# Performance work log

Measured on AMD Instinct MI355X. Metric: run time of the kernel, lower is better.

Reference implementation:

```python
import jax, jax.numpy as jnp
import numpy as np

TYPE_PANEL, TYPE_DIALOG, TYPE_CHAR = 1, 2, 3
NUM_ELEMS = 64  # max element index per type (panel count cap per page)
B, S, D = 8, 4096, 768
NPC, NDS = 4, 4  # num_panel_classes, num_dialog_shapes


def setup_inputs() -> dict:
    key = jax.random.key(0)
    ks = jax.random.split(key, 16)
    w = lambda k, shp: jax.random.normal(k, shp, dtype=jnp.float32) * 0.02
    return {
        "element_types": jax.random.randint(ks[0], (B, S), 0, 4, dtype=jnp.int32),
        "element_indices": jax.random.randint(ks[1], (B, S), 0, NUM_ELEMS, dtype=jnp.int32),
        "parent_panel_indices": jax.random.randint(ks[2], (B, S), 0, NUM_ELEMS, dtype=jnp.int32),
        "style_vector": jax.random.normal(ks[3], (B, 4), dtype=jnp.float32),
        "type_emb": w(ks[4], (4, D)),
        "index_emb": w(ks[5], (NUM_ELEMS, D)),
        "parent_emb": w(ks[6], (NUM_ELEMS, D)),
        "style_w": w(ks[7], (4, D)),
        "style_b": jnp.zeros((D,), jnp.float32),
        "ln_g": jnp.ones((D,), jnp.float32),
        "ln_b": jnp.zeros((D,), jnp.float32),
        "panel_w": w(ks[8], (D, NPC + 4)),
        "panel_b": jnp.zeros((NPC + 4,), jnp.float32),
        "dialog_w": w(ks[9], (2 * D, NDS + 4)),
        "dialog_b": jnp.zeros((NDS + 4,), jnp.float32),
        "char_w": w(ks[10], (2 * D, 4)),
        "char_b": jnp.zeros((4,), jnp.float32),
    }


def reference(element_types, element_indices, parent_panel_indices, style_vector,
              type_emb, index_emb, parent_emb, style_w, style_b, ln_g, ln_b,
              panel_w, panel_b, dialog_w, dialog_b, char_w, char_b):
    Bv, Sv = element_types.shape
    # --- TokenLayoutEncoder: embedding sum + style projection + LayerNorm ---
    x = type_emb[element_types] + index_emb[element_indices] + parent_emb[parent_panel_indices]
    x = x + (style_vector @ style_w + style_b)[:, None, :]
    mu = x.mean(-1, keepdims=True)
    var = ((x - mu) ** 2).mean(-1, keepdims=True)
    feats = (x - mu) * jax.lax.rsqrt(var + 1e-5) * ln_g + ln_b  # (B,S,D)

    # --- vectorized _build_parent_remap: orig panel idx -> kept panel order pos ---
    panel_mask = element_types == TYPE_PANEL                      # (B,S)
    kept = (jnp.cumsum(panel_mask, axis=1) - 1).astype(jnp.int32) # order pos of each panel token
    brow = jnp.arange(Bv, dtype=jnp.int32)[:, None]
    col = jnp.where(panel_mask, element_indices, NUM_ELEMS)       # dummy slot for non-panels
    remap = (jnp.full((Bv, NUM_ELEMS + 1), -1, jnp.int32)
             .at[brow, col].max(kept))[:, :NUM_ELEMS]             # (B, NUM_ELEMS)
    # kept panel order pos -> sequence position (for parent feature gather)
    slot = jnp.where(panel_mask, kept, Sv)
    seq_ids = jnp.broadcast_to(jnp.arange(Sv, dtype=jnp.int32), (Bv, Sv))
    pos_table = (jnp.zeros((Bv, Sv + 1), jnp.int32)
                 .at[brow, slot].set(seq_ids))[:, :Sv]            # (B,S)

    # --- parent_pos per token (DIALOG/CHAR only), -1 otherwise ---
    child_mask = (element_types == TYPE_DIALOG) | (element_types == TYPE_CHAR)
    ppos = jnp.where(child_mask,
                     jnp.take_along_axis(remap, parent_panel_indices, axis=1), -1)
    valid = ppos >= 0
    pseq = jnp.take_along_axis(pos_table, jnp.clip(ppos, 0, Sv - 1), axis=1)
    parent_feats = jnp.take_along_axis(feats, pseq[..., None], axis=1)
    parent_feats = parent_feats * valid[..., None].astype(feats.dtype)
    cat = jnp.concatenate([feats, parent_feats], axis=-1)         # (B,S,2D)

    # --- ParallelPredictionHeads, masked per token type ---
    panel_out = (feats @ panel_w + panel_b) * panel_mask[..., None].astype(feats.dtype)
    dmask = ((element_types == TYPE_DIALOG) & valid)[..., None].astype(feats.dtype)
    cmask = ((element_types == TYPE_CHAR) & valid)[..., None].astype(feats.dtype)
    dialog_out = (cat @ dialog_w + dialog_b) * dmask
    char_out = (cat @ char_w + char_b) * cmask
    return panel_out, dialog_out, char_out
```

## Files before the change

### kernel.cpp

```cpp
#include <hip/hip_runtime.h>

#define NB 8
#define NS 4096
#define ND 768

typedef float4 f4;

static __device__ __forceinline__ float wred(float v) {
    v += __shfl_xor(v, 32, 64);
    v += __shfl_xor(v, 16, 64);
    v += __shfl_xor(v, 8, 64);
    v += __shfl_xor(v, 4, 64);
    v += __shfl_xor(v, 2, 64);
    v += __shfl_xor(v, 1, 64);
    return v;
}

static __device__ __forceinline__ f4 ld4(const float* __restrict__ p, int i) {
    return ((const f4*)p)[i];
}

__global__ __launch_bounds__(256) void lp_pre(
    const int* __restrict__ et, const int* __restrict__ ei,
    const float* __restrict__ sv, const float* __restrict__ sw,
    const float* __restrict__ sb,
    int* __restrict__ table, float* __restrict__ sprj)
{
    if (blockIdx.x < 128) {
        int t = blockIdx.x * 256 + threadIdx.x;
        if (et[t] == 1) {
            int b = t >> 12;
            atomicMax(&table[b * 64 + ei[t]], t & (NS - 1));
        }
    } else {
        const int lane = threadIdx.x & 63;
        const int b = (blockIdx.x - 128) * 4 + (threadIdx.x >> 6);
        const float sv0 = sv[b*4+0], sv1 = sv[b*4+1], sv2 = sv[b*4+2], sv3 = sv[b*4+3];
        #pragma unroll
        for (int g = 0; g < 3; ++g) {
            int i = g*64 + lane;
            f4 w0 = ld4(sw, i), w1 = ld4(sw, 192+i), w2 = ld4(sw, 384+i), w3 = ld4(sw, 576+i);
            f4 bb = ld4(sb, i);
            f4 r;
            r.x = bb.x + sv0*w0.x + sv1*w1.x + sv2*w2.x + sv3*w3.x;
            r.y = bb.y + sv0*w0.y + sv1*w1.y + sv2*w2.y + sv3*w3.y;
            r.z = bb.z + sv0*w0.z + sv1*w1.z + sv2*w2.z + sv3*w3.z;
            r.w = bb.w + sv0*w0.w + sv1*w1.w + sv2*w2.w + sv3*w3.w;
            ((f4*)(sprj + b*ND))[i] = r;
        }
    }
}

__global__ __launch_bounds__(256) void lp_parent(
    const int* __restrict__ ei, const int* __restrict__ ppi,
    const float* __restrict__ temb, const float* __restrict__ iemb,
    const float* __restrict__ pemb, const float* __restrict__ lng,
    const float* __restrict__ lnb,
    const int* __restrict__ table, const float* __restrict__ sprj,
    float* __restrict__ pfeat)
{
    const int lane = threadIdx.x & 63;
    const int slot = blockIdx.x * 4 + (threadIdx.x >> 6);
    const int b = slot >> 6;
    const int pp = table[slot];
    if (pp < 0) return;
    const int ptok = b * NS + pp;
    const int pei = ei[ptok], pppi = ppi[ptok];
    const float* ie = iemb + pei * ND;
    const float* pe = pemb + pppi * ND;
    const float* sp = sprj + b * ND;

    f4 x[3]; float s1 = 0.f;
    #pragma unroll
    for (int g = 0; g < 3; ++g) {
        int i = g*64 + lane;
        f4 a = ld4(temb + ND, i), c = ld4(ie, i), d = ld4(pe, i), s = ld4(sp, i);
        x[g].x = a.x + c.x + d.x + s.x;
        x[g].y = a.y + c.y + d.y + s.y;
        x[g].z = a.z + c.z + d.z + s.z;
        x[g].w = a.w + c.w + d.w + s.w;
        s1 += x[g].x + x[g].y + x[g].z + x[g].w;
    }
    float mu = wred(s1) * (1.f/ND);
    float s2 = 0.f;
    #pragma unroll
    for (int g = 0; g < 3; ++g) {
        float dx = x[g].x-mu, dy = x[g].y-mu, dz = x[g].z-mu, dw_ = x[g].w-mu;
        s2 += dx*dx + dy*dy + dz*dz + dw_*dw_;
    }
    float rs = rsqrtf(wred(s2) * (1.f/ND) + 1e-5f);
    float* dst = pfeat + (size_t)slot * ND;
    #pragma unroll
    for (int g = 0; g < 3; ++g) {
        int i = g*64 + lane;
        f4 gg = ld4(lng, i), bb = ld4(lnb, i);
        f4 r;
        r.x = (x[g].x-mu)*rs*gg.x + bb.x;
        r.y = (x[g].y-mu)*rs*gg.y + bb.y;
        r.z = (x[g].z-mu)*rs*gg.z + bb.z;
        r.w = (x[g].w-mu)*rs*gg.w + bb.w;
        ((f4*)dst)[i] = r;
    }
}

__global__ __launch_bounds__(256) void lp_main(
    const int* __restrict__ et, const int* __restrict__ ei, const int* __restrict__ ppi,
    const float* __restrict__ temb, const float* __restrict__ iemb,
    const float* __restrict__ pemb, const float* __restrict__ lng,
    const float* __restrict__ lnb,
    const float* __restrict__ pw, const float* __restrict__ pb,
    const float* __restrict__ dw, const float* __restrict__ db,
    const float* __restrict__ cw, const float* __restrict__ cb,
    const int* __restrict__ table, const float* __restrict__ sprj,
    const float* __restrict__ pfeat,
    float* __restrict__ out)
{
    __shared__ float lds[4][2*ND];
    const int lane = threadIdx.x & 63;
    const int widx = threadIdx.x >> 6;
    const int t = blockIdx.x * 4 + widx;
    const int b = t >> 12;
    const int type = et[t];

    float pval = 0.f, dval = 0.f, cval = 0.f;

    if (type != 0) {
        const int my_ei = ei[t], my_ppi = ppi[t];
        float* fl = lds[widx];
        const float* te = temb + type * ND;
        const float* ie = iemb + my_ei * ND;
        const float* pe = pemb + my_ppi * ND;
        const float* sp = sprj + b * ND;

        f4 x[3]; float s1 = 0.f;
        #pragma unroll
        for (int g = 0; g < 3; ++g) {
            int i = g*64 + lane;
            f4 a = ld4(te, i), c = ld4(ie, i), d = ld4(pe, i), s = ld4(sp, i);
            x[g].x = a.x + c.x + d.x + s.x;
            x[g].y = a.y + c.y + d.y + s.y;
            x[g].z = a.z + c.z + d.z + s.z;
            x[g].w = a.w + c.w + d.w + s.w;
            s1 += x[g].x + x[g].y + x[g].z + x[g].w;
        }
        float mu = wred(s1) * (1.f/ND);
        float s2 = 0.f;
        #pragma unroll
        for (int g = 0; g < 3; ++g) {
            float dx = x[g].x-mu, dy = x[g].y-mu, dz = x[g].z-mu, dw_ = x[g].w-mu;
            s2 += dx*dx + dy*dy + dz*dz + dw_*dw_;
        }
        float rs = rsqrtf(wred(s2) * (1.f/ND) + 1e-5f);
        #pragma unroll
        for (int g = 0; g < 3; ++g) {
            int i = g*64 + lane;
            f4 gg = ld4(lng, i), bb = ld4(lnb, i);
            f4 r;
            r.x = (x[g].x-mu)*rs*gg.x + bb.x;
            r.y = (x[g].y-mu)*rs*gg.y + bb.y;
            r.z = (x[g].z-mu)*rs*gg.z + bb.z;
            r.w = (x[g].w-mu)*rs*gg.w + bb.w;
            ((f4*)fl)[i] = r;
        }

        if (type == 1) {
            const int di = lane >> 3;
            float acc = 0.f;
            #pragma unroll 16
            for (int s = 0; s < 96; ++s)
                acc += pw[s*64 + lane] * fl[s*8 + di];
            acc += __shfl_xor(acc, 8, 64);
            acc += __shfl_xor(acc, 16, 64);
            acc += __shfl_xor(acc, 32, 64);
            pval = acc + pb[lane & 7];
        } else {
            const int pp = table[b*64 + my_ppi];
            if (pp >= 0) {
                const float* pfr = pfeat + (size_t)(b*64 + my_ppi) * ND;
                #pragma unroll
                for (int g = 0; g < 3; ++g)
                    ((f4*)(fl + ND))[g*64 + lane] = ld4(pfr, g*64 + lane);

                if (type == 2) {
                    const int di = lane >> 3;
                    float acc = 0.f;
                    #pragma unroll 16
                    for (int s = 0; s < 192; ++s)
                        acc += dw[s*64 + lane] * fl[s*8 + di];
                    acc += __shfl_xor(acc, 8, 64);
                    acc += __shfl_xor(acc, 16, 64);
                    acc += __shfl_xor(acc, 32, 64);
                    dval = acc + db[lane & 7];
                } else {
                    const int di = lane >> 2;
                    float acc = 0.f;
                    #pragma unroll 16
                    for (int s = 0; s < 96; ++s)
                        acc += cw[s*64 + lane] * fl[s*16 + di];
                    acc += __shfl_xor(acc, 4, 64);
                    acc += __shfl_xor(acc, 8, 64);
                    acc += __shfl_xor(acc, 16, 64);
                    acc += __shfl_xor(acc, 32, 64);
                    cval = acc + cb[lane & 3];
                }
            }
        }
    }

    if (lane < 8) out[(size_t)t*8 + lane] = pval;
    if (lane < 8) out[(size_t)NB*NS*8 + (size_t)t*8 + lane] = dval;
    if (lane < 4) out[(size_t)NB*NS*16 + (size_t)t*4 + lane] = cval;
}

extern "C" void kernel_launch(void* const* d_in, const int* in_sizes, int n_in,
                              void* d_out, int out_size, void* d_ws, size_t ws_size,
                              hipStream_t stream) {
    const int* et  = (const int*)d_in[0];
    const int* ei  = (const int*)d_in[1];
    const int* ppi = (const int*)d_in[2];
    const float* sv   = (const float*)d_in[3];
    const float* temb = (const float*)d_in[4];
    const float* iemb = (const float*)d_in[5];
    const float* pemb = (const float*)d_in[6];
    const float* sw   = (const float*)d_in[7];
    const float* sb   = (const float*)d_in[8];
    const float* lng  = (const float*)d_in[9];
    const float* lnb  = (const float*)d_in[10];
    const float* pw   = (const float*)d_in[11];
    const float* pb   = (const float*)d_in[12];
    const float* dw   = (const float*)d_in[13];
    const float* db   = (const float*)d_in[14];
    const float* cw   = (const float*)d_in[15];
    const float* cbp  = (const float*)d_in[16];
    float* out = (float*)d_out;

    int*   table = (int*)d_ws;
    float* sprj  = (float*)((char*)d_ws + 4096);
    float* pfeat = (float*)((char*)d_ws + 32768);

    hipMemsetAsync(table, 0xFF, NB * 64 * sizeof(int), stream);

    lp_pre<<<130, 256, 0, stream>>>(et, ei, sv, sw, sb, table, sprj);
    lp_parent<<<128, 256, 0, stream>>>(ei, ppi, temb, iemb, pemb, lng, lnb,
                                       table, sprj, pfeat);
    lp_main<<<(NB*NS)/4, 256, 0, stream>>>(et, ei, ppi, temb, iemb, pemb,
                                           lng, lnb, pw, pb, dw, db, cw, cbp,
                                           table, sprj, pfeat, out);
}
```

Baseline: 137.5 us.

## Recompute parent features inline and transpose head weights for register dot products

Drops the separate parent-feature kernel and has each dialog/char token recompute its parent panel's LayerNorm features inline. The pre-kernel now also transposes the head weights into output-major float4 layouts, so the main kernel computes all head outputs per lane in registers and reduces them with shuffles instead of staging features in LDS. LayerNorm switches to single-pass sum and sum-of-squares, and each wave's outputs are written as float4 stores from a single lane. This removes a kernel launch and LDS round trips, at the cost of redundant parent recomputation, more registers, and slightly less numerically stable variance.

```diff
diff --git a/kernel.cpp b/kernel.cpp
--- a/kernel.cpp
+++ b/kernel.cpp
@@ -6,35 +6,36 @@
 
 typedef float4 f4;
 
-static __device__ __forceinline__ float wred(float v) {
-    v += __shfl_xor(v, 32, 64);
-    v += __shfl_xor(v, 16, 64);
-    v += __shfl_xor(v, 8, 64);
-    v += __shfl_xor(v, 4, 64);
-    v += __shfl_xor(v, 2, 64);
-    v += __shfl_xor(v, 1, 64);
-    return v;
-}
-
 static __device__ __forceinline__ f4 ld4(const float* __restrict__ p, int i) {
     return ((const f4*)p)[i];
+}
+
+static __device__ __forceinline__ void dot4(float& acc, const f4& a, const f4& w) {
+    acc = fmaf(a.x, w.x, acc);
+    acc = fmaf(a.y, w.y, acc);
+    acc = fmaf(a.z, w.z, acc);
+    acc = fmaf(a.w, w.w, acc);
 }
 
 __global__ __launch_bounds__(256) void lp_pre(
     const int* __restrict__ et, const int* __restrict__ ei,
     const float* __restrict__ sv, const float* __restrict__ sw,
     const float* __restrict__ sb,
-    int* __restrict__ table, float* __restrict__ sprj)
+    const float* __restrict__ pw, const float* __restrict__ dw,
+    const float* __restrict__ cw,
+    int* __restrict__ table, float* __restrict__ sprj,
+    float* __restrict__ pwx, float* __restrict__ dwx, float* __restrict__ cwx)
 {
-    if (blockIdx.x < 128) {
-        int t = blockIdx.x * 256 + threadIdx.x;
+    const int bx = blockIdx.x;
+    if (bx < 128) {
+        int t = bx * 256 + threadIdx.x;
         if (et[t] == 1) {
             int b = t >> 12;
             atomicMax(&table[b * 64 + ei[t]], t & (NS - 1));
         }
-    } else {
+    } else if (bx < 130) {
         const int lane = threadIdx.x & 63;
-        const int b = (blockIdx.x - 128) * 4 + (threadIdx.x >> 6);
+        const int b = (bx - 128) * 4 + (threadIdx.x >> 6);
         const float sv0 = sv[b*4+0], sv1 = sv[b*4+1], sv2 = sv[b*4+2], sv3 = sv[b*4+3];
         #pragma unroll
         for (int g = 0; g < 3; ++g) {
@@ -48,58 +49,35 @@
             r.w = bb.w + sv0*w0.w + sv1*w1.w + sv2*w2.w + sv3*w3.w;
             ((f4*)(sprj + b*ND))[i] = r;
         }
-    }
-}
-
-__global__ __launch_bounds__(256) void lp_parent(
-    const int* __restrict__ ei, const int* __restrict__ ppi,
-    const float* __restrict__ temb, const float* __restrict__ iemb,
-    const float* __restrict__ pemb, const float* __restrict__ lng,
-    const float* __restrict__ lnb,
-    const int* __restrict__ table, const float* __restrict__ sprj,
-    float* __restrict__ pfeat)
-{
-    const int lane = threadIdx.x & 63;
-    const int slot = blockIdx.x * 4 + (threadIdx.x >> 6);
-    const int b = slot >> 6;
-    const int pp = table[slot];
-    if (pp < 0) return;
-    const int ptok = b * NS + pp;
-    const int pei = ei[ptok], pppi = ppi[ptok];
-    const float* ie = iemb + pei * ND;
-    const float* pe = pemb + pppi * ND;
-    const float* sp = sprj + b * ND;
-
-    f4 x[3]; float s1 = 0.f;
-    #pragma unroll
-    for (int g = 0; g < 3; ++g) {
-        int i = g*64 + lane;
-        f4 a = ld4(temb + ND, i), c = ld4(ie, i), d = ld4(pe, i), s = ld4(sp, i);
-        x[g].x = a.x + c.x + d.x + s.x;
-        x[g].y = a.y + c.y + d.y + s.y;
-        x[g].z = a.z + c.z + d.z + s.z;
-        x[g].w = a.w + c.w + d.w + s.w;
-        s1 += x[g].x + x[g].y + x[g].z + x[g].w;
-    }
-    float mu = wred(s1) * (1.f/ND);
-    float s2 = 0.f;
-    #pragma unroll
-    for (int g = 0; g < 3; ++g) {
-        float dx = x[g].x-mu, dy = x[g].y-mu, dz = x[g].z-mu, dw_ = x[g].w-mu;
-        s2 += dx*dx + dy*dy + dz*dz + dw_*dw_;
-    }
-    float rs = rsqrtf(wred(s2) * (1.f/ND) + 1e-5f);
-    float* dst = pfeat + (size_t)slot * ND;
-    #pragma unroll
-    for (int g = 0; g < 3; ++g) {
-        int i = g*64 + lane;
-        f4 gg = ld4(lng, i), bb = ld4(lnb, i);
+    } else {
+        const int q = (bx - 130) * 256 + threadIdx.x;
         f4 r;
-        r.x = (x[g].x-mu)*rs*gg.x + bb.x;
-        r.y = (x[g].y-mu)*rs*gg.y + bb.y;
-        r.z = (x[g].z-mu)*rs*gg.z + bb.z;
-        r.w = (x[g].w-mu)*rs*gg.w + bb.w;
-        ((f4*)dst)[i] = r;
+        if (q < 1536) {
+            int o = q / 192, i = q - o * 192, d0 = 4 * i;
+            r.x = pw[(d0+0)*8 + o];
+            r.y = pw[(d0+1)*8 + o];
+            r.z = pw[(d0+2)*8 + o];
+            r.w = pw[(d0+3)*8 + o];
+            ((f4*)pwx)[q] = r;
+        } else if (q < 4608) {
+            int u = q - 1536;
+            int o = u / 384, i = u - o * 384;
+            int d0 = (i < 192) ? 4*i : 768 + 4*(i - 192);
+            r.x = dw[(d0+0)*8 + o];
+            r.y = dw[(d0+1)*8 + o];
+            r.z = dw[(d0+2)*8 + o];
+            r.w = dw[(d0+3)*8 + o];
+            ((f4*)dwx)[u] = r;
+        } else {
+            int u = q - 4608;
+            int o = u / 384, i = u - o * 384;
+            int d0 = (i < 192) ? 4*i : 768 + 4*(i - 192);
+            r.x = cw[(d0+0)*4 + o];
+            r.y = cw[(d0+1)*4 + o];
+            r.z = cw[(d0+2)*4 + o];
+            r.w = cw[(d0+3)*4 + o];
+            ((f4*)cwx)[u] = r;
+        }
     }
 }
 
@@ -108,108 +86,196 @@
     const float* __restrict__ temb, const float* __restrict__ iemb,
     const float* __restrict__ pemb, const float* __restrict__ lng,
     const float* __restrict__ lnb,
-    const float* __restrict__ pw, const float* __restrict__ pb,
-    const float* __restrict__ dw, const float* __restrict__ db,
-    const float* __restrict__ cw, const float* __restrict__ cb,
+    const float* __restrict__ pb, const float* __restrict__ db,
+    const float* __restrict__ cb,
     const int* __restrict__ table, const float* __restrict__ sprj,
-    const float* __restrict__ pfeat,
+    const float* __restrict__ pwx, const float* __restrict__ dwx,
+    const float* __restrict__ cwx,
     float* __restrict__ out)
 {
-    __shared__ float lds[4][2*ND];
     const int lane = threadIdx.x & 63;
-    const int widx = threadIdx.x >> 6;
-    const int t = blockIdx.x * 4 + widx;
+    const int t = blockIdx.x * 4 + (threadIdx.x >> 6);
     const int b = t >> 12;
     const int type = et[t];
 
-    float pval = 0.f, dval = 0.f, cval = 0.f;
+    f4 z4; z4.x = 0.f; z4.y = 0.f; z4.z = 0.f; z4.w = 0.f;
+    f4 po0 = z4, po1 = z4, dq0 = z4, dq1 = z4, cq0 = z4;
 
     if (type != 0) {
         const int my_ei = ei[t], my_ppi = ppi[t];
-        float* fl = lds[widx];
+        const int pp = table[b * 64 + my_ppi];
+        const int ptokc = b * NS + (pp > 0 ? pp : 0);
+        const int pei = ei[ptokc], pppi = ppi[ptokc];
+
         const float* te = temb + type * ND;
         const float* ie = iemb + my_ei * ND;
         const float* pe = pemb + my_ppi * ND;
         const float* sp = sprj + b * ND;
 
-        f4 x[3]; float s1 = 0.f;
+        f4 x[3], xs[3];
+        float s1 = 0.f, sq = 0.f;
         #pragma unroll
         for (int g = 0; g < 3; ++g) {
-            int i = g*64 + lane;
+            int i = g * 64 + lane;
             f4 a = ld4(te, i), c = ld4(ie, i), d = ld4(pe, i), s = ld4(sp, i);
-            x[g].x = a.x + c.x + d.x + s.x;
-            x[g].y = a.y + c.y + d.y + s.y;
-            x[g].z = a.z + c.z + d.z + s.z;
-            x[g].w = a.w + c.w + d.w + s.w;
-            s1 += x[g].x + x[g].y + x[g].z + x[g].w;
-        }
-        float mu = wred(s1) * (1.f/ND);
-        float s2 = 0.f;
-        #pragma unroll
-        for (int g = 0; g < 3; ++g) {
-            float dx = x[g].x-mu, dy = x[g].y-mu, dz = x[g].z-mu, dw_ = x[g].w-mu;
-            s2 += dx*dx + dy*dy + dz*dz + dw_*dw_;
-        }
-        float rs = rsqrtf(wred(s2) * (1.f/ND) + 1e-5f);
-        #pragma unroll
-        for (int g = 0; g < 3; ++g) {
-            int i = g*64 + lane;
-            f4 gg = ld4(lng, i), bb = ld4(lnb, i);
-            f4 r;
-            r.x = (x[g].x-mu)*rs*gg.x + bb.x;
-            r.y = (x[g].y-mu)*rs*gg.y + bb.y;
-            r.z = (x[g].z-mu)*rs*gg.z + bb.z;
-            r.w = (x[g].w-mu)*rs*gg.w + bb.w;
-            ((f4*)fl)[i] = r;
+            xs[g] = s;
+            f4 v;
+            v.x = a.x + c.x + d.x + s.x;
+            v.y = a.y + c.y + d.y + s.y;
+            v.z = a.z + c.z + d.z + s.z;
+            v.w = a.w + c.w + d.w + s.w;
+            x[g] = v;
+            s1 += v.x + v.y + v.z + v.w;
+            sq = fmaf(v.x, v.x, sq);
+            sq = fmaf(v.y, v.y, sq);
+            sq = fmaf(v.z, v.z, sq);
+            sq = fmaf(v.w, v.w, sq);
         }
 
         if (type == 1) {
-            const int di = lane >> 3;
-            float acc = 0.f;
-            #pragma unroll 16
-            for (int s = 0; s < 96; ++s)
-                acc += pw[s*64 + lane] * fl[s*8 + di];
-            acc += __shfl_xor(acc, 8, 64);
-            acc += __shfl_xor(acc, 16, 64);
-            acc += __shfl_xor(acc, 32, 64);
-            pval = acc + pb[lane & 7];
-        } else {
-            const int pp = table[b*64 + my_ppi];
-            if (pp >= 0) {
-                const float* pfr = pfeat + (size_t)(b*64 + my_ppi) * ND;
-                #pragma unroll
-                for (int g = 0; g < 3; ++g)
-                    ((f4*)(fl + ND))[g*64 + lane] = ld4(pfr, g*64 + lane);
-
-                if (type == 2) {
-                    const int di = lane >> 3;
-                    float acc = 0.f;
-                    #pragma unroll 16
-                    for (int s = 0; s < 192; ++s)
-                        acc += dw[s*64 + lane] * fl[s*8 + di];
-                    acc += __shfl_xor(acc, 8, 64);
-                    acc += __shfl_xor(acc, 16, 64);
-                    acc += __shfl_xor(acc, 32, 64);
-                    dval = acc + db[lane & 7];
-                } else {
-                    const int di = lane >> 2;
-                    float acc = 0.f;
-                    #pragma unroll 16
-                    for (int s = 0; s < 96; ++s)
-                        acc += cw[s*64 + lane] * fl[s*16 + di];
-                    acc += __shfl_xor(acc, 4, 64);
-                    acc += __shfl_xor(acc, 8, 64);
-                    acc += __shfl_xor(acc, 16, 64);
-                    acc += __shfl_xor(acc, 32, 64);
-                    cval = acc + cb[lane & 3];
+            #pragma unroll
+            for (int k = 32; k >= 1; k >>= 1) {
+                s1 += __shfl_xor(s1, k, 64);
+                sq += __shfl_xor(sq, k, 64);
+            }
+            float mu = s1 * (1.f / ND);
+            float rs = rsqrtf(sq * (1.f / ND) - mu * mu + 1e-5f);
+            float c0 = -mu * rs;
+            #pragma unroll
+            for (int g = 0; g < 3; ++g) {
+                int i = g * 64 + lane;
+                f4 gg = ld4(lng, i), bb = ld4(lnb, i);
+                f4 v = x[g], xn;
+                xn.x = fmaf(v.x, rs, c0); v.x = fmaf(xn.x, gg.x, bb.x);
+                xn.y = fmaf(v.y, rs, c0); v.y = fmaf(xn.y, gg.y, bb.y);
+                xn.z = fmaf(v.z, rs, c0); v.z = fmaf(xn.z, gg.z, bb.z);
+                xn.w = fmaf(v.w, rs, c0); v.w = fmaf(xn.w, gg.w, bb.w);
+                x[g] = v;
+            }
+            float acc[8];
+            #pragma unroll
+            for (int o = 0; o < 8; ++o) acc[o] = 0.f;
+            #pragma unroll
+            for (int g = 0; g < 3; ++g) {
+                int i = g * 64 + lane;
+                #pragma unroll
+                for (int o = 0; o < 8; ++o)
+                    dot4(acc[o], x[g], ld4(pwx, o * 192 + i));
+            }
+            #pragma unroll
+            for (int k = 32; k >= 1; k >>= 1) {
+                #pragma unroll
+                for (int o = 0; o < 8; ++o)
+                    acc[o] += __shfl_xor(acc[o], k, 64);
+            }
+            po0.x = acc[0] + pb[0]; po0.y = acc[1] + pb[1];
+            po0.z = acc[2] + pb[2]; po0.w = acc[3] + pb[3];
+            po1.x = acc[4] + pb[4]; po1.y = acc[5] + pb[5];
+            po1.z = acc[6] + pb[6]; po1.w = acc[7] + pb[7];
+        } else if (pp >= 0) {
+            const float* ie2 = iemb + pei * ND;
+            const float* pe2 = pemb + pppi * ND;
+            f4 xp[3];
+            float s1p = 0.f, sqp = 0.f;
+            #pragma unroll
+            for (int g = 0; g < 3; ++g) {
+                int i = g * 64 + lane;
+                f4 a = ld4(temb + ND, i), c = ld4(ie2, i), d = ld4(pe2, i);
+                f4 v;
+                v.x = a.x + c.x + d.x + xs[g].x;
+                v.y = a.y + c.y + d.y + xs[g].y;
+                v.z = a.z + c.z + d.z + xs[g].z;
+                v.w = a.w + c.w + d.w + xs[g].w;
+                xp[g] = v;
+                s1p += v.x + v.y + v.z + v.w;
+                sqp = fmaf(v.x, v.x, sqp);
+                sqp = fmaf(v.y, v.y, sqp);
+                sqp = fmaf(v.z, v.z, sqp);
+                sqp = fmaf(v.w, v.w, sqp);
+            }
+            #pragma unroll
+            for (int k = 32; k >= 1; k >>= 1) {
+                s1  += __shfl_xor(s1,  k, 64);
+                sq  += __shfl_xor(sq,  k, 64);
+                s1p += __shfl_xor(s1p, k, 64);
+                sqp += __shfl_xor(sqp, k, 64);
+            }
+            float mu  = s1  * (1.f / ND);
+            float rs  = rsqrtf(sq  * (1.f / ND) - mu  * mu  + 1e-5f);
+            float mup = s1p * (1.f / ND);
+            float rsp = rsqrtf(sqp * (1.f / ND) - mup * mup + 1e-5f);
+            float c0 = -mu * rs, c0p = -mup * rsp;
+            #pragma unroll
+            for (int g = 0; g < 3; ++g) {
+                int i = g * 64 + lane;
+                f4 gg = ld4(lng, i), bb = ld4(lnb, i);
+                f4 v = x[g], w = xp[g], xn;
+                xn.x = fmaf(v.x, rs, c0); v.x = fmaf(xn.x, gg.x, bb.x);
+                xn.y = fmaf(v.y, rs, c0); v.y = fmaf(xn.y, gg.y, bb.y);
+                xn.z = fmaf(v.z, rs, c0); v.z = fmaf(xn.z, gg.z, bb.z);
+                xn.w = fmaf(v.w, rs, c0); v.w = fmaf(xn.w, gg.w, bb.w);
+                x[g] = v;
+                xn.x = fmaf(w.x, rsp, c0p); w.x = fmaf(xn.x, gg.x, bb.x);
+                xn.y = fmaf(w.y, rsp, c0p); w.y = fmaf(xn.y, gg.y, bb.y);
+                xn.z = fmaf(w.z, rsp, c0p); w.z = fmaf(xn.z, gg.z, bb.z);
+                xn.w = fmaf(w.w, rsp, c0p); w.w = fmaf(xn.w, gg.w, bb.w);
+                xp[g] = w;
+            }
+            if (type == 2) {
+                float acc[8];
+                #pragma unroll
+                for (int o = 0; o < 8; ++o) acc[o] = 0.f;
+                #pragma unroll
+                for (int g = 0; g < 3; ++g) {
+                    int i = g * 64 + lane;
+                    #pragma unroll
+                    for (int o = 0; o < 8; ++o) {
+                        dot4(acc[o], x[g],  ld4(dwx, o * 384 + i));
+                        dot4(acc[o], xp[g], ld4(dwx, o * 384 + 192 + i));
+                    }
                 }
+                #pragma unroll
+                for (int k = 32; k >= 1; k >>= 1) {
+                    #pragma unroll
+                    for (int o = 0; o < 8; ++o)
+                        acc[o] += __shfl_xor(acc[o], k, 64);
+                }
+                dq0.x = acc[0] + db[0]; dq0.y = acc[1] + db[1];
+                dq0.z = acc[2] + db[2]; dq0.w = acc[3] + db[3];
+                dq1.x = acc[4] + db[4]; dq1.y = acc[5] + db[5];
+                dq1.z = acc[6] + db[6]; dq1.w = acc[7] + db[7];
+            } else {
+                float acc[4];
+                #pragma unroll
+                for (int o = 0; o < 4; ++o) acc[o] = 0.f;
+                #pragma unroll
+                for (int g = 0; g < 3; ++g) {
+                    int i = g * 64 + lane;
+                    #pragma unroll
+                    for (int o = 0; o < 4; ++o) {
+                        dot4(acc[o], x[g],  ld4(cwx, o * 384 + i));
+                        dot4(acc[o], xp[g], ld4(cwx, o * 384 + 192 + i));
+                    }
+                }
+                #pragma unroll
+                for (int k = 32; k >= 1; k >>= 1) {
+                    #pragma unroll
+                    for (int o = 0; o < 4; ++o)
+                        acc[o] += __shfl_xor(acc[o], k, 64);
+                }
+                cq0.x = acc[0] + cb[0]; cq0.y = acc[1] + cb[1];
+                cq0.z = acc[2] + cb[2]; cq0.w = acc[3] + cb[3];
             }
         }
     }
 
-    if (lane < 8) out[(size_t)t*8 + lane] = pval;
-    if (lane < 8) out[(size_t)NB*NS*8 + (size_t)t*8 + lane] = dval;
-    if (lane < 4) out[(size_t)NB*NS*16 + (size_t)t*4 + lane] = cval;
+    if (lane == 0) {
+        f4* op = (f4*)(out + (size_t)t * 8);
+        op[0] = po0; op[1] = po1;
+        f4* od = (f4*)(out + (size_t)NB * NS * 8 + (size_t)t * 8);
+        od[0] = dq0; od[1] = dq1;
+        ((f4*)(out + (size_t)NB * NS * 16 + (size_t)t * 4))[0] = cq0;
+    }
 }
 
 extern "C" void kernel_launch(void* const* d_in, const int* in_sizes, int n_in,
@@ -236,14 +302,15 @@
 
     int*   table = (int*)d_ws;
     float* sprj  = (float*)((char*)d_ws + 4096);
-    float* pfeat = (float*)((char*)d_ws + 32768);
+    float* pwx   = (float*)((char*)d_ws + 32768);
+    float* dwx   = (float*)((char*)d_ws + 32768 + 24576);
+    float* cwx   = (float*)((char*)d_ws + 32768 + 24576 + 49152);
 
     hipMemsetAsync(table, 0xFF, NB * 64 * sizeof(int), stream);
 
-    lp_pre<<<130, 256, 0, stream>>>(et, ei, sv, sw, sb, table, sprj);
-    lp_parent<<<128, 256, 0, stream>>>(ei, ppi, temb, iemb, pemb, lng, lnb,
-                                       table, sprj, pfeat);
+    lp_pre<<<154, 256, 0, stream>>>(et, ei, sv, sw, sb, pw, dw, cw,
+                                    table, sprj, pwx, dwx, cwx);
     lp_main<<<(NB*NS)/4, 256, 0, stream>>>(et, ei, ppi, temb, iemb, pemb,
-                                           lng, lnb, pw, pb, dw, db, cw, cbp,
-                                           table, sprj, pfeat, out);
-}
+                                           lng, lnb, pb, db, cbp,
+                                           table, sprj, pwx, dwx, cwx, out);
+}
```

Measured after the change: 149.8 us. 9.0% more time.
